# Performance work log

Measured on AMD Instinct MI355X. Metric: run time of the kernel, lower is better.

## Reference

```python
import jax, jax.numpy as jnp
import numpy as np

K = 3
STRIDE = 1
PADDING = 1


def _conv2d(x, w, b, stride, padding):
    out = jax.lax.conv_general_dilated(
        x, w, window_strides=(stride, stride),
        padding=[(padding, padding), (padding, padding)],
        dimension_numbers=('NCHW', 'OIHW', 'NCHW'))
    return out + b[None, :, None, None]


def _grid_sample_bilinear_zeros(x, grid):
    B, C, Hin, Win = x.shape
    gx = (grid[..., 0] + 1.0) * (Win * 0.5) - 0.5  # (B,Hg,Wg) pixel coords
    gy = (grid[..., 1] + 1.0) * (Hin * 0.5) - 0.5
    x0f = jnp.floor(gx)
    y0f = jnp.floor(gy)
    wx1 = gx - x0f  # bilinear weights
    wy1 = gy - y0f
    x0 = x0f.astype(jnp.int32)
    y0 = y0f.astype(jnp.int32)
    xf = x.reshape(B, C, Hin * Win)

    def gather(yi, xi):
        valid = (xi >= 0) & (xi < Win) & (yi >= 0) & (yi < Hin)  # zero padding
        idx = jnp.clip(yi, 0, Hin - 1) * Win + jnp.clip(xi, 0, Win - 1)
        g = jax.vmap(lambda xb, ib: xb[:, ib])(xf, idx)  # (B,C,Hg,Wg)
        return g * valid[:, None, :, :].astype(x.dtype)

    w00 = ((1.0 - wx1) * (1.0 - wy1))[:, None]
    w01 = (wx1 * (1.0 - wy1))[:, None]
    w10 = ((1.0 - wx1) * wy1)[:, None]
    w11 = (wx1 * wy1)[:, None]
    return (gather(y0, x0) * w00 + gather(y0, x0 + 1) * w01 +
            gather(y0 + 1, x0) * w10 + gather(y0 + 1, x0 + 1) * w11)


def setup_inputs() -> dict:
    key = jax.random.key(0)
    k1, k2, k3 = jax.random.split(key, 3)
    B, C, O, H, W = 8, 128, 128, 64, 64
    x = jax.random.normal(k1, (B, C, H, W), dtype=jnp.float32)
    # small offset-predictor weights so sampled locations stay near the grid
    w_off = jax.random.normal(k2, (2 * K * K, C, K, K), dtype=jnp.float32) * 1e-3
    b_off = jnp.zeros((2 * K * K,), dtype=jnp.float32)
    w_main = jax.random.normal(k3, (O, C, K, K), dtype=jnp.float32) * 0.05
    b_main = jnp.zeros((O,), dtype=jnp.float32)
    return {"x": x, "w_off": w_off, "b_off": b_off, "w_main": w_main, "b_main": b_main}


def reference(x, w_off, b_off, w_main, b_main):
    offset = _conv2d(x, w_off, b_off, STRIDE, PADDING)  # (B, 2*K*K, H, W)
    B, _, H, W = offset.shape
    off = jnp.transpose(offset, (0, 2, 3, 1)).reshape(B, H, W, K, K, 2)
    # The torch in-place loops reduce to:
    #   x-comp: cumsum over i of column j=0, broadcast over j
    #   y-comp: cumsum over j of row    i=0, broadcast over i
    ox = jnp.cumsum(off[:, :, :, :, 0, 0], axis=3)  # (B,H,W,K)
    oy = jnp.cumsum(off[:, :, :, 0, :, 1], axis=3)  # (B,H,W,K)
    ox_f = jnp.broadcast_to(ox[..., None], (B, H, W, K, K))
    oy_f = jnp.broadcast_to(oy[:, :, :, None, :], (B, H, W, K, K))
    off_f = jnp.stack([ox_f, oy_f], axis=-1).reshape(B, H, W, K * K, 2)

    y_range = jnp.linspace(-1.0, 1.0, H, dtype=x.dtype)
    x_range = jnp.linspace(-1.0, 1.0, W, dtype=x.dtype)
    yg, xg = jnp.meshgrid(y_range, x_range, indexing='ij')
    base = jnp.stack((xg, yg), axis=-1)  # (H,W,2)
    grid = base[None, :, :, None, :] + off_f  # (B,H,W,K*K,2)
    grid = grid.reshape(B, H, W * K * K, 2)

    xs = _grid_sample_bilinear_zeros(x, grid)  # (B,C,H,W*K*K)
    C = x.shape[1]
    xs = xs.reshape(B, C, H, W, K * K)
    wm = w_main.reshape(w_main.shape[0], C, K * K)
    out = jnp.einsum('bchwk,ock->bohw', xs, wm)
    return out + b_main[None, :, None, None]
```

## Files before the change

### kernel.cpp

```cpp
#include <hip/hip_runtime.h>
#include <hip/hip_bf16.h>
#include <stdint.h>

typedef unsigned short u16;
typedef unsigned int u32;
typedef __attribute__((ext_vector_type(8))) short short8;
typedef __attribute__((ext_vector_type(4))) float float4v;

#define CH 128
#define OO 128
#define KD 1152

__device__ __forceinline__ u16 f2bf(float v) {
    __hip_bfloat16 h = __float2bfloat16(v);
    return *reinterpret_cast<u16*>(&h);
}
__device__ __forceinline__ float bf_lo(u32 u) { u32 t = u << 16;         return __builtin_bit_cast(float, t); }
__device__ __forceinline__ float bf_hi(u32 u) { u32 t = u & 0xffff0000u; return __builtin_bit_cast(float, t); }
__device__ __forceinline__ u32 pack_bf16(float lo, float hi) {
    u32 ul = __builtin_bit_cast(u32, lo);
    u32 uh = __builtin_bit_cast(u32, hi);
    return ((ul + 0x8000u) >> 16) | ((uh + 0x8000u) & 0xffff0000u);
}

__global__ __launch_bounds__(256) void prep_kernel(const float* __restrict__ x,
                                                   const float* __restrict__ w_off,
                                                   const float* __restrict__ w_main,
                                                   __hip_bfloat16* __restrict__ xt,
                                                   float* __restrict__ partial,
                                                   u16* __restrict__ WbSwz) {
    __shared__ float st[64][65];
    int bid = blockIdx.x;
    int tid = threadIdx.x;
    if (bid < 512) {
        int b = bid >> 6;
        int h = bid & 63;
        const float* xb = x + ((size_t)b * CH) * 4096 + (size_t)h * 64;
        __hip_bfloat16* xo = xt + ((size_t)bid << 6) * CH;
        for (int cc0 = 0; cc0 < 128; cc0 += 64) {
            #pragma unroll
            for (int step = 0; step < 16; ++step) {
                int cl = (tid >> 6) + step * 4;
                int w = tid & 63;
                st[cl][w] = xb[(size_t)(cc0 + cl) * 4096 + w];
            }
            __syncthreads();
            #pragma unroll
            for (int step = 0; step < 16; ++step) {
                int w = (tid >> 6) + step * 4;
                int cl = tid & 63;
                xo[(size_t)w * CH + cc0 + cl] = __float2bfloat16(st[cl][w]);
            }
            __syncthreads();
        }
    } else if (bid < 1024) {
        int mb = (bid - 512) & 127;
        int chunk = (bid - 512) >> 7;
        int m = mb * 256 + tid;
        int b = m >> 12;
        int hw = m & 4095;
        int h = hw >> 6;
        int w = hw & 63;
        float acc[6] = {0.f, 0.f, 0.f, 0.f, 0.f, 0.f};
        int c0 = chunk * 32;
        for (int c = c0; c < c0 + 32; ++c) {
            const float* xc = x + ((size_t)(b * CH + c) << 12);
            float xv[9];
            #pragma unroll
            for (int dy = 0; dy < 3; ++dy) {
                int yy = h + dy - 1;
                bool vy = (unsigned)yy < 64u;
                #pragma unroll
                for (int dx = 0; dx < 3; ++dx) {
                    int xx = w + dx - 1;
                    bool vv = vy && ((unsigned)xx < 64u);
                    xv[dy * 3 + dx] = vv ? xc[yy * 64 + xx] : 0.f;
                }
            }
            const float* wbp = w_off + (size_t)c * 9;
            #pragma unroll
            for (int s = 0; s < 6; ++s) {
                int chn = (s < 3) ? s * 6 : (s - 3) * 2 + 1;
                const float* wp = wbp + (size_t)chn * (CH * 9);
                float a = acc[s];
                #pragma unroll
                for (int t = 0; t < 9; ++t) a = fmaf(xv[t], wp[t], a);
                acc[s] = a;
            }
        }
        float* po = partial + ((size_t)(chunk << 15) + m) * 6;
        #pragma unroll
        for (int s = 0; s < 6; ++s) po[s] = acc[s];
    } else {
        int unit = (bid - 1024) * 256 + tid;
        int lane6 = unit & 63;
        int t = (unit >> 6) & 7;
        int kc = unit >> 9;
        int o = t * 16 + (lane6 & 15);
        int q8 = (lane6 >> 4) * 8;
        int tap = kc >> 2;
        int cb = (kc & 3) * 32 + q8;
        u16 v8[8];
        #pragma unroll
        for (int j = 0; j < 8; ++j)
            v8[j] = f2bf(w_main[(size_t)o * KD + (cb + j) * 9 + tap]);
        *(uint4*)(WbSwz + (size_t)unit * 8) = *(const uint4*)v8;
    }
}

__global__ __launch_bounds__(256, 2) void fused_gemm_kernel(const __hip_bfloat16* __restrict__ xt,
                                                            const float* __restrict__ partial,
                                                            const float* __restrict__ b_off,
                                                            const u16* __restrict__ WbSwz,
                                                            const float* __restrict__ b_main,
                                                            float* __restrict__ out) {
    __shared__ __align__(16) u16 lA[16384];

    int tid = threadIdx.x;
    int wave = tid >> 6;
    int lane = tid & 63;
    int col = lane & 15;
    int q8 = (lane >> 4) * 8;
    int pbw = blockIdx.x * 64 + wave * 16;
    int m = pbw + col;
    int bimg = m >> 12;
    int h = (m & 4095) >> 6;
    int w = m & 63;

    float o6[6];
    #pragma unroll
    for (int s = 0; s < 6; ++s) {
        int chn = (s < 3) ? s * 6 : (s - 3) * 2 + 1;
        float v = b_off[chn];
        #pragma unroll
        for (int q = 0; q < 4; ++q) v += partial[((size_t)(q << 15) + m) * 6 + s];
        o6[s] = v;
    }
    float ox0 = o6[0], ox1 = ox0 + o6[1], ox2 = ox1 + o6[2];
    float oy0 = o6[3], oy1 = oy0 + o6[4], oy2 = oy1 + o6[5];
    const float step = 2.0f / 63.0f;
    float bxn = -1.0f + w * step;
    float byn = -1.0f + h * step;
    float gx0 = fmaf(bxn + ox0, 32.0f, 31.5f);
    float gx1 = fmaf(bxn + ox1, 32.0f, 31.5f);
    float gx2 = fmaf(bxn + ox2, 32.0f, 31.5f);
    float gy0 = fmaf(byn + oy0, 32.0f, 31.5f);
    float gy1 = fmaf(byn + oy1, 32.0f, 31.5f);
    float gy2 = fmaf(byn + oy2, 32.0f, 31.5f);

    const u32* xb = (const u32*)(xt + (((size_t)bimg << 12) * CH));

    float4v acc[8];
    #pragma unroll
    for (int t = 0; t < 8; ++t) acc[t] = (float4v){0.f, 0.f, 0.f, 0.f};

    for (int tap = 0; tap < 9; ++tap) {
        __syncthreads();
        const uint4* s4 = (const uint4*)(WbSwz + (size_t)tap * 16384);
        uint4* d4 = (uint4*)lA;
        #pragma unroll
        for (int it = 0; it < 8; ++it) d4[it * 256 + tid] = s4[it * 256 + tid];
        __syncthreads();

        float gxi = (tap >= 6) ? gx2 : ((tap >= 3) ? gx1 : gx0);
        int jm = tap - ((tap >= 6) ? 6 : ((tap >= 3) ? 3 : 0));
        float gyj = (jm == 2) ? gy2 : ((jm == 1) ? gy1 : gy0);
        float x0f = floorf(gxi), y0f = floorf(gyj);
        float wx = gxi - x0f, wy = gyj - y0f;
        int ix0 = (int)x0f, iy0 = (int)y0f;
        int ix1 = ix0 + 1, iy1 = iy0 + 1;
        float fx0 = ((unsigned)ix0 < 64u) ? 1.f : 0.f;
        float fx1 = ((unsigned)ix1 < 64u) ? 1.f : 0.f;
        float fy0 = ((unsigned)iy0 < 64u) ? 1.f : 0.f;
        float fy1 = ((unsigned)iy1 < 64u) ? 1.f : 0.f;
        float w00 = (1.f - wy) * (1.f - wx) * fy0 * fx0;
        float w01 = (1.f - wy) * wx * fy0 * fx1;
        float w10 = wy * (1.f - wx) * fy1 * fx0;
        float w11 = wy * wx * fy1 * fx1;
        int cx0 = min(max(ix0, 0), 63), cx1 = min(max(ix1, 0), 63);
        int cy0 = min(max(iy0, 0), 63), cy1 = min(max(iy1, 0), 63);
        int r00 = (cy0 * 64 + cx0) * CH + q8;
        int r01 = (cy0 * 64 + cx1) * CH + q8;
        int r10 = (cy1 * 64 + cx0) * CH + q8;
        int r11 = (cy1 * 64 + cx1) * CH + q8;

        #pragma unroll
        for (int cc = 0; cc < 4; ++cc) {
            int co = cc * 16;
            uint4 u00 = *(const uint4*)(xb + (r00 >> 1) + co);
            uint4 u01 = *(const uint4*)(xb + (r01 >> 1) + co);
            uint4 u10 = *(const uint4*)(xb + (r10 >> 1) + co);
            uint4 u11 = *(const uint4*)(xb + (r11 >> 1) + co);
            const u32* p00 = (const u32*)&u00;
            const u32* p01 = (const u32*)&u01;
            const u32* p10 = (const u32*)&u10;
            const u32* p11 = (const u32*)&u11;
            u32 bp[4];
            #pragma unroll
            for (int qq = 0; qq < 4; ++qq) {
                float lo = w00 * bf_lo(p00[qq]);
                lo = fmaf(w01, bf_lo(p01[qq]), lo);
                lo = fmaf(w10, bf_lo(p10[qq]), lo);
                lo = fmaf(w11, bf_lo(p11[qq]), lo);
                float hi = w00 * bf_hi(p00[qq]);
                hi = fmaf(w01, bf_hi(p01[qq]), hi);
                hi = fmaf(w10, bf_hi(p10[qq]), hi);
                hi = fmaf(w11, bf_hi(p11[qq]), hi);
                bp[qq] = pack_bf16(lo, hi);
            }
            short8 bfrag = *(const short8*)bp;
            #pragma unroll
            for (int t = 0; t < 8; ++t) {
                short8 af = *(const short8*)&lA[((cc * 8 + t) * 64 + lane) * 8];
                acc[t] = __builtin_amdgcn_mfma_f32_16x16x32_bf16(af, bfrag, acc[t], 0, 0, 0);
            }
        }
    }

    int quad4 = (lane >> 4) * 4;
    int rem = m & 4095;
    #pragma unroll
    for (int t = 0; t < 8; ++t) {
        int ob = t * 16 + quad4;
        float4 bm = *(const float4*)(b_main + ob);
        float* op = out + (((size_t)(bimg * OO + ob)) << 12) + rem;
        op[0] = acc[t][0] + bm.x;
        op[4096] = acc[t][1] + bm.y;
        op[8192] = acc[t][2] + bm.z;
        op[12288] = acc[t][3] + bm.w;
    }
}

extern "C" void kernel_launch(void* const* d_in, const int* in_sizes, int n_in,
                              void* d_out, int out_size, void* d_ws, size_t ws_size,
                              hipStream_t stream) {
    const float* x      = (const float*)d_in[0];
    const float* w_off  = (const float*)d_in[1];
    const float* b_off  = (const float*)d_in[2];
    const float* w_main = (const float*)d_in[3];
    const float* b_main = (const float*)d_in[4];
    float* out = (float*)d_out;

    char* ws = (char*)d_ws;
    __hip_bfloat16* xt = (__hip_bfloat16*)ws;
    float* partial = (float*)(ws + 8388608);
    u16* WbSwz = (u16*)(ws + 8388608 + 3145728);

    prep_kernel<<<1096, 256, 0, stream>>>(x, w_off, w_main, xt, partial, WbSwz);
    fused_gemm_kernel<<<512, 256, 0, stream>>>(xt, partial, b_off, WbSwz, b_main, out);
}
```

Baseline: 141.1 us.

## Split taps across two waves per pixel tile and read weights from global

```diff
diff --git a/kernel.cpp b/kernel.cpp
--- a/kernel.cpp
+++ b/kernel.cpp
@@ -108,22 +108,23 @@
     }
 }
 
-__global__ __launch_bounds__(256, 2) void fused_gemm_kernel(const __hip_bfloat16* __restrict__ xt,
+__global__ __launch_bounds__(128, 4) void fused_gemm_kernel(const __hip_bfloat16* __restrict__ xt,
                                                             const float* __restrict__ partial,
                                                             const float* __restrict__ b_off,
                                                             const u16* __restrict__ WbSwz,
                                                             const float* __restrict__ b_main,
                                                             float* __restrict__ out) {
-    __shared__ __align__(16) u16 lA[16384];
+    __shared__ float4v red[2][4][64];
 
     int tid = threadIdx.x;
     int wave = tid >> 6;
     int lane = tid & 63;
     int col = lane & 15;
     int q8 = (lane >> 4) * 8;
-    int pbw = blockIdx.x * 64 + wave * 16;
-    int m = pbw + col;
-    int bimg = m >> 12;
+    int img = blockIdx.x & 7;
+    int tile = blockIdx.x >> 3;
+    int pb = img * 4096 + tile * 16;
+    int m = pb + col;
     int h = (m & 4095) >> 6;
     int w = m & 63;
 
@@ -148,20 +149,13 @@
     float gy1 = fmaf(byn + oy1, 32.0f, 31.5f);
     float gy2 = fmaf(byn + oy2, 32.0f, 31.5f);
 
-    const u32* xb = (const u32*)(xt + (((size_t)bimg << 12) * CH));
+    const u32* xb = (const u32*)(xt + (((size_t)img << 12) * CH));
 
     float4v acc[8];
     #pragma unroll
     for (int t = 0; t < 8; ++t) acc[t] = (float4v){0.f, 0.f, 0.f, 0.f};
 
-    for (int tap = 0; tap < 9; ++tap) {
-        __syncthreads();
-        const uint4* s4 = (const uint4*)(WbSwz + (size_t)tap * 16384);
-        uint4* d4 = (uint4*)lA;
-        #pragma unroll
-        for (int it = 0; it < 8; ++it) d4[it * 256 + tid] = s4[it * 256 + tid];
-        __syncthreads();
-
+    auto process_tap = [&](int tap, int ccb, int ncc) {
         float gxi = (tap >= 6) ? gx2 : ((tap >= 3) ? gx1 : gx0);
         int jm = tap - ((tap >= 6) ? 6 : ((tap >= 3) ? 3 : 0));
         float gyj = (jm == 2) ? gy2 : ((jm == 1) ? gy1 : gy0);
@@ -179,18 +173,19 @@
         float w11 = wy * wx * fy1 * fx1;
         int cx0 = min(max(ix0, 0), 63), cx1 = min(max(ix1, 0), 63);
         int cy0 = min(max(iy0, 0), 63), cy1 = min(max(iy1, 0), 63);
-        int r00 = (cy0 * 64 + cx0) * CH + q8;
-        int r01 = (cy0 * 64 + cx1) * CH + q8;
-        int r10 = (cy1 * 64 + cx0) * CH + q8;
-        int r11 = (cy1 * 64 + cx1) * CH + q8;
-
-        #pragma unroll
-        for (int cc = 0; cc < 4; ++cc) {
+        int r00 = ((cy0 * 64 + cx0) * CH + q8) >> 1;
+        int r01 = ((cy0 * 64 + cx1) * CH + q8) >> 1;
+        int r10 = ((cy1 * 64 + cx0) * CH + q8) >> 1;
+        int r11 = ((cy1 * 64 + cx1) * CH + q8) >> 1;
+
+        #pragma unroll 4
+        for (int q = 0; q < ncc; ++q) {
+            int cc = ccb + q;
             int co = cc * 16;
-            uint4 u00 = *(const uint4*)(xb + (r00 >> 1) + co);
-            uint4 u01 = *(const uint4*)(xb + (r01 >> 1) + co);
-            uint4 u10 = *(const uint4*)(xb + (r10 >> 1) + co);
-            uint4 u11 = *(const uint4*)(xb + (r11 >> 1) + co);
+            uint4 u00 = *(const uint4*)(xb + r00 + co);
+            uint4 u01 = *(const uint4*)(xb + r01 + co);
+            uint4 u10 = *(const uint4*)(xb + r10 + co);
+            uint4 u11 = *(const uint4*)(xb + r11 + co);
             const u32* p00 = (const u32*)&u00;
             const u32* p01 = (const u32*)&u01;
             const u32* p10 = (const u32*)&u10;
@@ -209,21 +204,37 @@
                 bp[qq] = pack_bf16(lo, hi);
             }
             short8 bfrag = *(const short8*)bp;
+            const u16* Ap = WbSwz + ((size_t)((tap * 4 + cc) * 512 + lane) * 8);
             #pragma unroll
             for (int t = 0; t < 8; ++t) {
-                short8 af = *(const short8*)&lA[((cc * 8 + t) * 64 + lane) * 8];
+                short8 af = *(const short8*)(Ap + (size_t)t * 512);
                 acc[t] = __builtin_amdgcn_mfma_f32_16x16x32_bf16(af, bfrag, acc[t], 0, 0, 0);
             }
         }
+    };
+
+    int t0 = wave ? 5 : 0;
+    for (int tt = 0; tt < 4; ++tt) process_tap(t0 + tt, 0, 4);
+    process_tap(4, wave * 2, 2);
+
+    #pragma unroll
+    for (int s = 0; s < 4; ++s)
+        red[wave][s][lane] = acc[wave ? s : 4 + s];
+    __syncthreads();
+    #pragma unroll
+    for (int s = 0; s < 4; ++s) {
+        if (wave == 0) acc[s] += red[1][s][lane];
+        else           acc[4 + s] += red[0][s][lane];
     }
 
     int quad4 = (lane >> 4) * 4;
     int rem = m & 4095;
     #pragma unroll
-    for (int t = 0; t < 8; ++t) {
+    for (int s = 0; s < 4; ++s) {
+        int t = wave * 4 + s;
         int ob = t * 16 + quad4;
         float4 bm = *(const float4*)(b_main + ob);
-        float* op = out + (((size_t)(bimg * OO + ob)) << 12) + rem;
+        float* op = out + (((size_t)(img * OO + ob)) << 12) + rem;
         op[0] = acc[t][0] + bm.x;
         op[4096] = acc[t][1] + bm.y;
         op[8192] = acc[t][2] + bm.z;
@@ -247,5 +258,5 @@
     u16* WbSwz = (u16*)(ws + 8388608 + 3145728);
 
     prep_kernel<<<1096, 256, 0, stream>>>(x, w_off, w_main, xt, partial, WbSwz);
-    fused_gemm_kernel<<<512, 256, 0, stream>>>(xt, partial, b_off, WbSwz, b_main, out);
-}
+    fused_gemm_kernel<<<2048, 128, 0, stream>>>(xt, partial, b_off, WbSwz, b_main, out);
+}
```

Measured after the change: 303.1 us. 2.15x slower.
